# Performance work log

Hardware: AMD Instinct MI355X
Metric: run time of the kernel (lower is better)

## Reference

```python
import jax, jax.numpy as jnp
import numpy as np
from jax import lax

OC, IC, K = 256, 256, 3
PAD, STRIDE = 1, 1
NNZ = 59000
N, H, W = 32, 56, 56


def setup_inputs() -> dict:
    key = jax.random.key(0)
    k1, k2, k3, k4 = jax.random.split(key, 4)
    x = jax.random.normal(k1, (N, IC, H, W), dtype=jnp.float32)
    W_val = jax.random.normal(k2, (NNZ,), dtype=jnp.float32)
    W_idx = jax.random.randint(k3, (NNZ,), 0, OC * IC * K * K, dtype=jnp.int64)
    bias = jax.random.normal(k4, (OC,), dtype=jnp.float32)
    return {"x": x, "W_val": W_val, "W_idx": W_idx, "bias": bias}


def reference(x, W_val, W_idx, bias):
    # Scatter COO values into the dense [OC, IC, K, K] weight (duplicates sum).
    dense_w = jnp.zeros((OC * IC * K * K,), dtype=W_val.dtype).at[W_idx].add(W_val)
    dense_w = dense_w.reshape(OC, IC, K, K)
    # conv2d, NCHW / OIHW layout, stride=STRIDE, symmetric padding=PAD
    out = lax.conv_general_dilated(
        x, dense_w,
        window_strides=(STRIDE, STRIDE),
        padding=[(PAD, PAD), (PAD, PAD)],
        dimension_numbers=("NCHW", "OIHW", "NCHW"),
    )
    out = out + bias[None, :, None, None]
    return out
```

## Files before the change

### kernel.cpp

```cpp
#include <hip/hip_runtime.h>

typedef unsigned short ushort;
typedef __attribute__((ext_vector_type(8))) short bf16x8;
typedef __attribute__((ext_vector_type(4))) float f32x4;
typedef __attribute__((ext_vector_type(4))) ushort us4;

#define NBATCH 32
#define ICN 256
#define OCN 256
#define HSZ 56
#define WSZ 56
#define HP 58
#define SPAT (HP*HP)
#define KTOT 2304
#define MTOT (NBATCH*HSZ*WSZ)
#define NT   (KTOT/64)

#define XP_BYTES ((size_t)NBATCH*SPAT*ICN*2)
#define WD_BYTES ((size_t)OCN*KTOT*4)

__device__ __forceinline__ ushort f2bf(float f) {
  union { float f; unsigned u; } c; c.f = f;
  unsigned r = c.u + 0x7FFFu + ((c.u >> 16) & 1u);
  return (ushort)(r >> 16);
}

__global__ void k_transpose(const float* __restrict__ x, ushort* __restrict__ xp) {
  __shared__ ushort t2[WSZ*264];
  int h = blockIdx.x, n = blockIdx.y;
  ushort* dst = xp + ((size_t)n*SPAT + (size_t)h*HP)*ICN;
  if (h == 0 || h == HP-1) {
    for (int e = threadIdx.x; e < HP*ICN/4; e += 256) ((us4*)dst)[e] = (us4){0,0,0,0};
    return;
  }
  const float* src = x + ((size_t)n*ICN*HSZ*WSZ) + (size_t)(h-1)*WSZ;
  for (int e = threadIdx.x; e < ICN*WSZ; e += 256) {
    int ic = e / WSZ, w = e - ic*WSZ;
    t2[w*264 + ic] = f2bf(src[(size_t)ic*(HSZ*WSZ) + w]);
  }
  __syncthreads();
  for (int e4 = threadIdx.x; e4 < HP*ICN/4; e4 += 256) {
    int wp = e4 >> 6, ic4 = (e4 & 63) << 2;
    us4 v = (wp == 0 || wp == HP-1) ? (us4){0,0,0,0}
                                    : *(const us4*)&t2[(wp-1)*264 + ic4];
    ((us4*)dst)[e4] = v;
  }
}

__global__ void k_scatter(const int* __restrict__ idx, const float* __restrict__ val,
                          float* __restrict__ wd, int nnz) {
  int i = blockIdx.x*256 + threadIdx.x;
  if (i >= nnz) return;
  int id = idx[i];
  int oc = id / (ICN*9);
  int rem = id - oc*(ICN*9);
  int ic = rem / 9;
  int k9 = rem - ic*9;
  atomicAdd(wd + (size_t)oc*KTOT + k9*ICN + ic, val[i]);
}

__global__ void k_convert3(const float* __restrict__ wd, ushort* __restrict__ bm3) {
  int e = blockIdx.x*256 + threadIdx.x;
  int lam = e & 63;
  int f   = (e >> 6) & 3;
  int wc  = (e >> 8) & 3;
  int kh  = (e >> 10) & 1;
  int t   = e >> 11;
  int oc  = wc*64 + f*16 + (lam & 15);
  int k   = (t >> 2)*256 + (t & 3)*64 + kh*32 + (lam >> 4)*8;
  const float* src = wd + (size_t)oc*KTOT + k;
  float4 v0 = *(const float4*)(src);
  float4 v1 = *(const float4*)(src + 4);
  us4 lo, hi;
  lo[0]=f2bf(v0.x); lo[1]=f2bf(v0.y); lo[2]=f2bf(v0.z); lo[3]=f2bf(v0.w);
  hi[0]=f2bf(v1.x); hi[1]=f2bf(v1.y); hi[2]=f2bf(v1.z); hi[3]=f2bf(v1.w);
  ushort* dst = bm3 + (size_t)e*8;
  *(us4*)(dst) = lo; *(us4*)(dst+4) = hi;
}


#define GLD(gsrc, ldst) __builtin_amdgcn_global_load_lds( \
    (const __attribute__((address_space(1))) void*)(gsrc), \
    (__attribute__((address_space(3))) void*)(ldst), 16, 0, 0)
#define BAR()  asm volatile("s_barrier" ::: "memory")
#define VMW(N) do { asm volatile("s_waitcnt vmcnt(" #N ")" ::: "memory"); \
                    __builtin_amdgcn_sched_barrier(0); } while (0)
#define LGKM(N) do { asm volatile("s_waitcnt lgkmcnt(" #N ")" ::: "memory"); \
                     __builtin_amdgcn_sched_barrier(0); } while (0)

#define STAGE_AU(T1, U, BF) do { \
    const int t4_ = (T1) >> 2; const int khh_ = t4_/3, khw_ = t4_ - khh_*3; \
    const int koff_ = (khh_*HP + khw_)*256 + (((T1) & 3) << 6); \
    ushort* d_ = &Ab[(BF)*16384 + (U)*8192]; \
    GLD(xp + ((U) ? srcA10 : srcA00) + koff_, d_ + ldsOff0); \
    GLD(xp + ((U) ? srcA11 : srcA01) + koff_, d_ + ldsOff1); } while (0)

#define GLB(DST, VOFF) \
    asm volatile("global_load_dwordx4 %0, %4, %5 offset:0\n\t" \
                 "global_load_dwordx4 %1, %4, %5 offset:1024\n\t" \
                 "global_load_dwordx4 %2, %4, %5 offset:2048\n\t" \
                 "global_load_dwordx4 %3, %4, %5 offset:3072" \
                 : "=&v"(DST[0]), "=&v"(DST[1]), "=&v"(DST[2]), "=&v"(DST[3]) \
                 : "v"(VOFF), "s"(bm3) : "memory")

#define LOADA_TO(DST, KH, MH, BFB) do { \
    unsigned a_ = ((KH) ? aL1v : aL0v) + (unsigned)((BFB) + (MH)*8192); \
    asm volatile("ds_read_b128 %0, %4 offset:0\n\t" \
                 "ds_read_b128 %1, %4 offset:2048\n\t" \
                 "ds_read_b128 %2, %4 offset:4096\n\t" \
                 "ds_read_b128 %3, %4 offset:6144" \
                 : "=&v"(DST[0]), "=&v"(DST[1]), "=&v"(DST[2]), "=&v"(DST[3]) \
                 : "v"(a_)); } while (0)

#define MFMA16(MH, AV, BV) do { \
    __builtin_amdgcn_s_setprio(1); \
    _Pragma("unroll") \
    for (int f_ = 0; f_ < 4; ++f_) { \
      _Pragma("unroll") \
      for (int n_ = 0; n_ < 4; ++n_) \
        acc[(MH)*4+f_][n_] = __builtin_amdgcn_mfma_f32_16x16x32_bf16( \
            AV[f_], BV[n_], acc[(MH)*4+f_][n_], 0, 0, 0); \
    } \
    __builtin_amdgcn_s_setprio(0); } while (0)

__global__ __launch_bounds__(512, 2) void k_gemm8(const ushort* __restrict__ xp,
                                                  const ushort* __restrict__ bm3,
                                                  const float* __restrict__ bias,
                                                  float* __restrict__ out) {
  __shared__ __align__(128) ushort Ab[3*16384];

  const int tid = threadIdx.x;
  const int lam = tid & 63;
  const int wv  = tid >> 6;
  const int wr  = wv >> 2;
  const int wc  = wv & 3;
  const int la  = lam & 15;
  const int m0  = blockIdx.x * 256;

  const unsigned AbB = (unsigned)(uintptr_t)(__attribute__((address_space(3))) char*)Ab;

  const int q0 = (lam >> 4) ^ (la & 7);
  const unsigned aL0v = AbB + wr*16384 + la*128 + q0*16;
  const unsigned aL1v = AbB + wr*16384 + la*128 + (q0 ^ 4)*16;

  const unsigned wcB = wc*4096 + lam*16;

  const int ldsOff0 = (0*8 + wv)*512;
  const int ldsOff1 = (1*8 + wv)*512;
  int srcA00, srcA01, srcA10, srcA11;
  {
    const int oA = (lam & 7) ^ (lam >> 3);
    int m, n, rem, oh, ow, r;
    r = (0*8 + wv)*8 + (lam >> 3);
    m = m0 + 0*128 + r; n = m/3136; rem = m - n*3136; oh = rem/56; ow = rem - oh*56;
    srcA00 = (n*SPAT + oh*HP + ow)*ICN + oA*8;
    r = (1*8 + wv)*8 + (lam >> 3);
    m = m0 + 0*128 + r; n = m/3136; rem = m - n*3136; oh = rem/56; ow = rem - oh*56;
    srcA01 = (n*SPAT + oh*HP + ow)*ICN + oA*8;
    r = (0*8 + wv)*8 + (lam >> 3);
    m = m0 + 1*128 + r; n = m/3136; rem = m - n*3136; oh = rem/56; ow = rem - oh*56;
    srcA10 = (n*SPAT + oh*HP + ow)*ICN + oA*8;
    r = (1*8 + wv)*8 + (lam >> 3);
    m = m0 + 1*128 + r; n = m/3136; rem = m - n*3136; oh = rem/56; ow = rem - oh*56;
    srcA11 = (n*SPAT + oh*HP + ow)*ICN + oA*8;
  }

  f32x4 acc[8][4];
#pragma unroll
  for (int a = 0; a < 8; ++a)
#pragma unroll
    for (int b = 0; b < 4; ++b) acc[a][b] = (f32x4){0.f, 0.f, 0.f, 0.f};

  bf16x8 avq0_[4], avq1_[4], avq2_[4], avq3_[4], bvA_[4], bvB_[4];

  STAGE_AU(0, 0, 0); STAGE_AU(0, 1, 0);
  STAGE_AU(1, 0, 1); STAGE_AU(1, 1, 1);
  GLB(bvA_, wcB);
  VMW(4);
  BAR();
  LOADA_TO(avq0_, 0, 0, 0); LOADA_TO(avq1_, 0, 1, 0);

  int bf0 = 0, bf1 = 1, bf2 = 2;
  for (int t = 0; t < NT-2; ++t) {
    const int b0b = bf0*32768, b1b = bf1*32768;
    const unsigned vb = (unsigned)t*32768 + wcB;
    LOADA_TO(avq2_, 1, 0, b0b);
    GLB(bvB_, vb + 16384);
    VMW(4);
    LGKM(8);
    MFMA16(0, avq0_, bvA_);
    LOADA_TO(avq3_, 1, 1, b0b);
    STAGE_AU(t+2, 0, bf2);
    LGKM(8);
    MFMA16(1, avq1_, bvA_);
    BAR();
    LOADA_TO(avq0_, 0, 0, b1b);
    STAGE_AU(t+2, 1, bf2);
    VMW(4);
    LGKM(8);
    MFMA16(0, avq2_, bvB_);
    LOADA_TO(avq1_, 0, 1, b1b);
    GLB(bvA_, vb + 32768);
    LGKM(8);
    MFMA16(1, avq3_, bvB_);
    BAR();
    int bt = bf0; bf0 = bf1; bf1 = bf2; bf2 = bt;
  }

  {
    const int t = NT-2;
    const int b0b = bf0*32768, b1b = bf1*32768;
    const unsigned vb = (unsigned)t*32768 + wcB;
    LOADA_TO(avq2_, 1, 0, b0b);
    GLB(bvB_, vb + 16384);
    VMW(4);
    LGKM(8);
    MFMA16(0, avq0_, bvA_);
    LOADA_TO(avq3_, 1, 1, b0b);
    LGKM(8);
    MFMA16(1, avq1_, bvA_);
    BAR();
    LOADA_TO(avq0_, 0, 0, b1b);
    VMW(0);
    LGKM(8);
    MFMA16(0, avq2_, bvB_);
    LOADA_TO(avq1_, 0, 1, b1b);
    GLB(bvA_, vb + 32768);
    LGKM(8);
    MFMA16(1, avq3_, bvB_);
    BAR();
    int bt = bf0; bf0 = bf1; bf1 = bf2; bf2 = bt;
  }

  {
    const int t = NT-1;
    const int b0b = bf0*32768;
    const unsigned vb = (unsigned)t*32768 + wcB;
    LOADA_TO(avq2_, 1, 0, b0b);
    GLB(bvB_, vb + 16384);
    VMW(4);
    LGKM(8);
    MFMA16(0, avq0_, bvA_);
    LOADA_TO(avq3_, 1, 1, b0b);
    LGKM(8);
    MFMA16(1, avq1_, bvA_);
    VMW(0);
    LGKM(4);
    MFMA16(0, avq2_, bvB_);
    LGKM(0);
    MFMA16(1, avq3_, bvB_);
  }

#pragma unroll
  for (int nn = 0; nn < 4; ++nn) {
    int oc = wc*64 + nn*16 + la;
    float bvs = bias[oc];
#pragma unroll
    for (int mf = 0; mf < 8; ++mf) {
      int m = m0 + wr*128 + mf*16 + ((lam >> 4) << 2);
      int n = m / 3136;
      int rem = m - n*3136;
      float4 o;
      o.x = acc[mf][nn][0] + bvs;
      o.y = acc[mf][nn][1] + bvs;
      o.z = acc[mf][nn][2] + bvs;
      o.w = acc[mf][nn][3] + bvs;
      *(float4*)(out + ((size_t)(n*OCN + oc))*3136 + rem) = o;
    }
  }
}

extern "C" void kernel_launch(void* const* d_in, const int* in_sizes, int n_in,
                              void* d_out, int out_size, void* d_ws, size_t ws_size,
                              hipStream_t stream) {
  const float* x    = (const float*)d_in[0];
  const float* wval = (const float*)d_in[1];
  const int*   widx = (const int*)d_in[2];
  const float* bias = (const float*)d_in[3];
  float* out = (float*)d_out;
  const int nnz = in_sizes[1];

  char* ws = (char*)d_ws;
  ushort* xp  = (ushort*)ws;
  float*  wd  = (float*)(ws + XP_BYTES);
  ushort* bm3 = (ushort*)(ws + XP_BYTES + WD_BYTES);

  hipMemsetAsync(wd, 0, WD_BYTES, stream);
  k_transpose<<<dim3(HP, NBATCH), 256, 0, stream>>>(x, xp);
  k_scatter<<<dim3((nnz + 255)/256), 256, 0, stream>>>(widx, wval, wd, nnz);
  k_convert3<<<dim3((NT*2*16*64)/256), 256, 0, stream>>>(wd, bm3);
  k_gemm8<<<dim3(MTOT/256), 512, 0, stream>>>(xp, bm3, bias, out);
}
```

Baseline: 160.3 us.

## Switch GEMM inner loop from 16x16x32 to 32x32x16 bf16 MFMA tiles

Replaces the 16x16x32 MFMA micro-tiles with 32x32x16 MFMA instructions. This changes the weight pre-pack layout, the LDS staging layout (no XOR swizzle now), the A/B fragment loads and the epilogue store mapping. Larger MFMA tiles raise the compute per operand fetched and issue fewer instructions. The unswizzled LDS layout may cause bank conflicts on the ds_read_b128 fragment reads.

```diff
diff --git a/kernel.cpp b/kernel.cpp
--- a/kernel.cpp
+++ b/kernel.cpp
@@ -2,7 +2,7 @@
 
 typedef unsigned short ushort;
 typedef __attribute__((ext_vector_type(8))) short bf16x8;
-typedef __attribute__((ext_vector_type(4))) float f32x4;
+typedef __attribute__((ext_vector_type(16))) float f32x16;
 typedef __attribute__((ext_vector_type(4))) ushort us4;
 
 #define NBATCH 32
@@ -59,22 +59,21 @@
   atomicAdd(wd + (size_t)oc*KTOT + k9*ICN + ic, val[i]);
 }
 
-__global__ void k_convert3(const float* __restrict__ wd, ushort* __restrict__ bm3) {
+__global__ void k_convert4(const float* __restrict__ wd, ushort* __restrict__ bm4) {
   int e = blockIdx.x*256 + threadIdx.x;
-  int lam = e & 63;
-  int f   = (e >> 6) & 3;
-  int wc  = (e >> 8) & 3;
-  int kh  = (e >> 10) & 1;
-  int t   = e >> 11;
-  int oc  = wc*64 + f*16 + (lam & 15);
-  int k   = (t >> 2)*256 + (t & 3)*64 + kh*32 + (lam >> 4)*8;
+  int lam   = e & 63;
+  int nsubg = (e >> 6) & 7;
+  int ks    = (e >> 9) & 3;
+  int t     = e >> 11;
+  int oc = nsubg*32 + (lam & 31);
+  int k  = (t >> 2)*256 + (t & 3)*64 + ks*16 + (lam >> 5)*8;
   const float* src = wd + (size_t)oc*KTOT + k;
   float4 v0 = *(const float4*)(src);
   float4 v1 = *(const float4*)(src + 4);
   us4 lo, hi;
   lo[0]=f2bf(v0.x); lo[1]=f2bf(v0.y); lo[2]=f2bf(v0.z); lo[3]=f2bf(v0.w);
   hi[0]=f2bf(v1.x); hi[1]=f2bf(v1.y); hi[2]=f2bf(v1.z); hi[3]=f2bf(v1.w);
-  ushort* dst = bm3 + (size_t)e*8;
+  ushort* dst = bm4 + (size_t)e*8;
   *(us4*)(dst) = lo; *(us4*)(dst+4) = hi;
 }
 
@@ -88,43 +87,39 @@
 #define LGKM(N) do { asm volatile("s_waitcnt lgkmcnt(" #N ")" ::: "memory"); \
                      __builtin_amdgcn_sched_barrier(0); } while (0)
 
-#define STAGE_AU(T1, U, BF) do { \
-    const int t4_ = (T1) >> 2; const int khh_ = t4_/3, khw_ = t4_ - khh_*3; \
-    const int koff_ = (khh_*HP + khw_)*256 + (((T1) & 3) << 6); \
-    ushort* d_ = &Ab[(BF)*16384 + (U)*8192]; \
-    GLD(xp + ((U) ? srcA10 : srcA00) + koff_, d_ + ldsOff0); \
-    GLD(xp + ((U) ? srcA11 : srcA01) + koff_, d_ + ldsOff1); } while (0)
-
-#define GLB(DST, VOFF) \
-    asm volatile("global_load_dwordx4 %0, %4, %5 offset:0\n\t" \
-                 "global_load_dwordx4 %1, %4, %5 offset:1024\n\t" \
-                 "global_load_dwordx4 %2, %4, %5 offset:2048\n\t" \
-                 "global_load_dwordx4 %3, %4, %5 offset:3072" \
-                 : "=&v"(DST[0]), "=&v"(DST[1]), "=&v"(DST[2]), "=&v"(DST[3]) \
-                 : "v"(VOFF), "s"(bm3) : "memory")
-
-#define LOADA_TO(DST, KH, MH, BFB) do { \
-    unsigned a_ = ((KH) ? aL1v : aL0v) + (unsigned)((BFB) + (MH)*8192); \
+#define STAGE2(T2, HALF, B2B) do { \
+    const int t4_ = (T2) >> 2; const int khh_ = t4_/3, khw_ = t4_ - khh_*3; \
+    const int koff_ = (khh_*HP + khw_)*256 + (((T2) & 3) << 6); \
+    ushort* d_ = (ushort*)((char*)Ab + (B2B)); \
+    GLD(xp + ((HALF) ? sA2 : sA0) + koff_, d_ + dOffB + (HALF)*1024); \
+    GLD(xp + ((HALF) ? sA3 : sA1) + koff_, d_ + dOffB + (HALF)*1024 + 512); } while (0)
+
+#define GLB2(D0, D1, VOFF) \
+    asm volatile("global_load_dwordx4 %0, %2, %3 offset:0\n\t" \
+                 "global_load_dwordx4 %1, %2, %3 offset:1024" \
+                 : "=&v"(D0), "=&v"(D1) \
+                 : "v"(VOFF), "s"(bm4) : "memory")
+
+#define LOADA(DST, KS, BFB) do { \
+    unsigned a_ = aBase + (unsigned)((BFB) + (KS)*4096); \
     asm volatile("ds_read_b128 %0, %4 offset:0\n\t" \
-                 "ds_read_b128 %1, %4 offset:2048\n\t" \
-                 "ds_read_b128 %2, %4 offset:4096\n\t" \
-                 "ds_read_b128 %3, %4 offset:6144" \
+                 "ds_read_b128 %1, %4 offset:1024\n\t" \
+                 "ds_read_b128 %2, %4 offset:2048\n\t" \
+                 "ds_read_b128 %3, %4 offset:3072" \
                  : "=&v"(DST[0]), "=&v"(DST[1]), "=&v"(DST[2]), "=&v"(DST[3]) \
                  : "v"(a_)); } while (0)
 
-#define MFMA16(MH, AV, BV) do { \
+#define MFMA32B(AVQ, B0, B1) do { \
     __builtin_amdgcn_s_setprio(1); \
     _Pragma("unroll") \
-    for (int f_ = 0; f_ < 4; ++f_) { \
-      _Pragma("unroll") \
-      for (int n_ = 0; n_ < 4; ++n_) \
-        acc[(MH)*4+f_][n_] = __builtin_amdgcn_mfma_f32_16x16x32_bf16( \
-            AV[f_], BV[n_], acc[(MH)*4+f_][n_], 0, 0, 0); \
+    for (int m_ = 0; m_ < 4; ++m_) { \
+      acc[m_*2+0] = __builtin_amdgcn_mfma_f32_32x32x16_bf16(AVQ[m_], B0, acc[m_*2+0], 0, 0, 0); \
+      acc[m_*2+1] = __builtin_amdgcn_mfma_f32_32x32x16_bf16(AVQ[m_], B1, acc[m_*2+1], 0, 0, 0); \
     } \
     __builtin_amdgcn_s_setprio(0); } while (0)
 
 __global__ __launch_bounds__(512, 2) void k_gemm8(const ushort* __restrict__ xp,
-                                                  const ushort* __restrict__ bm3,
+                                                  const ushort* __restrict__ bm4,
                                                   const float* __restrict__ bias,
                                                   float* __restrict__ out) {
   __shared__ __align__(128) ushort Ab[3*16384];
@@ -134,138 +129,136 @@
   const int wv  = tid >> 6;
   const int wr  = wv >> 2;
   const int wc  = wv & 3;
-  const int la  = lam & 15;
   const int m0  = blockIdx.x * 256;
 
   const unsigned AbB = (unsigned)(uintptr_t)(__attribute__((address_space(3))) char*)Ab;
 
-  const int q0 = (lam >> 4) ^ (la & 7);
-  const unsigned aL0v = AbB + wr*16384 + la*128 + q0*16;
-  const unsigned aL1v = AbB + wr*16384 + la*128 + (q0 ^ 4)*16;
-
-  const unsigned wcB = wc*4096 + lam*16;
-
-  const int ldsOff0 = (0*8 + wv)*512;
-  const int ldsOff1 = (1*8 + wv)*512;
-  int srcA00, srcA01, srcA10, srcA11;
+  const unsigned aBase = AbB + wr*16384 + lam*16;
+  const unsigned wcB = wc*2048 + lam*16;
+
+  const int dOffB = ((wv >> 2)*16 + (wv & 3)*4)*512;
+  int sA0, sA1, sA2, sA3;
   {
-    const int oA = (lam & 7) ^ (lam >> 3);
-    int m, n, rem, oh, ow, r;
-    r = (0*8 + wv)*8 + (lam >> 3);
-    m = m0 + 0*128 + r; n = m/3136; rem = m - n*3136; oh = rem/56; ow = rem - oh*56;
-    srcA00 = (n*SPAT + oh*HP + ow)*ICN + oA*8;
-    r = (1*8 + wv)*8 + (lam >> 3);
-    m = m0 + 0*128 + r; n = m/3136; rem = m - n*3136; oh = rem/56; ow = rem - oh*56;
-    srcA01 = (n*SPAT + oh*HP + ow)*ICN + oA*8;
-    r = (0*8 + wv)*8 + (lam >> 3);
-    m = m0 + 1*128 + r; n = m/3136; rem = m - n*3136; oh = rem/56; ow = rem - oh*56;
-    srcA10 = (n*SPAT + oh*HP + ow)*ICN + oA*8;
-    r = (1*8 + wv)*8 + (lam >> 3);
-    m = m0 + 1*128 + r; n = m/3136; rem = m - n*3136; oh = rem/56; ow = rem - oh*56;
-    srcA11 = (n*SPAT + oh*HP + ow)*ICN + oA*8;
-  }
-
-  f32x4 acc[8][4];
-#pragma unroll
-  for (int a = 0; a < 8; ++a)
-#pragma unroll
-    for (int b = 0; b < 4; ++b) acc[a][b] = (f32x4){0.f, 0.f, 0.f, 0.f};
-
-  bf16x8 avq0_[4], avq1_[4], avq2_[4], avq3_[4], bvA_[4], bvB_[4];
-
-  STAGE_AU(0, 0, 0); STAGE_AU(0, 1, 0);
-  STAGE_AU(1, 0, 1); STAGE_AU(1, 1, 1);
-  GLB(bvA_, wcB);
-  VMW(4);
+    const int kpart = (wv & 3)*16 + (lam >> 5)*8;
+    int m, n, rem, oh, ow;
+    m = m0 + (wv >> 2)*128 + 0*32 + (lam & 31);
+    n = m/3136; rem = m - n*3136; oh = rem/56; ow = rem - oh*56;
+    sA0 = (n*SPAT + oh*HP + ow)*ICN + kpart;
+    m = m0 + (wv >> 2)*128 + 1*32 + (lam & 31);
+    n = m/3136; rem = m - n*3136; oh = rem/56; ow = rem - oh*56;
+    sA1 = (n*SPAT + oh*HP + ow)*ICN + kpart;
+    m = m0 + (wv >> 2)*128 + 2*32 + (lam & 31);
+    n = m/3136; rem = m - n*3136; oh = rem/56; ow = rem - oh*56;
+    sA2 = (n*SPAT + oh*HP + ow)*ICN + kpart;
+    m = m0 + (wv >> 2)*128 + 3*32 + (lam & 31);
+    n = m/3136; rem = m - n*3136; oh = rem/56; ow = rem - oh*56;
+    sA3 = (n*SPAT + oh*HP + ow)*ICN + kpart;
+  }
+
+  f32x16 acc[8];
+#pragma unroll
+  for (int a = 0; a < 8; ++a) acc[a] = (f32x16)(0.f);
+
+  bf16x8 avq0_[4], avq1_[4], avq2_[4], avq3_[4];
+  bf16x8 bA0_, bA1_, bA2_, bA3_, bB0_, bB1_, bB2_, bB3_;
+
+  STAGE2(0, 0, 0); STAGE2(0, 1, 0);
+  STAGE2(1, 0, 32768); STAGE2(1, 1, 32768);
+  GLB2(bA0_, bA1_, wcB);
+  GLB2(bA2_, bA3_, wcB + 8192);
+  VMW(8);
   BAR();
-  LOADA_TO(avq0_, 0, 0, 0); LOADA_TO(avq1_, 0, 1, 0);
-
-  int bf0 = 0, bf1 = 1, bf2 = 2;
+  LOADA(avq0_, 0, 0); LOADA(avq1_, 1, 0);
+
+  int bf0b = 0, bf1b = 32768, bf2b = 65536;
   for (int t = 0; t < NT-2; ++t) {
-    const int b0b = bf0*32768, b1b = bf1*32768;
     const unsigned vb = (unsigned)t*32768 + wcB;
-    LOADA_TO(avq2_, 1, 0, b0b);
-    GLB(bvB_, vb + 16384);
-    VMW(4);
-    LGKM(8);
-    MFMA16(0, avq0_, bvA_);
-    LOADA_TO(avq3_, 1, 1, b0b);
-    STAGE_AU(t+2, 0, bf2);
-    LGKM(8);
-    MFMA16(1, avq1_, bvA_);
-    BAR();
-    LOADA_TO(avq0_, 0, 0, b1b);
-    STAGE_AU(t+2, 1, bf2);
-    VMW(4);
-    LGKM(8);
-    MFMA16(0, avq2_, bvB_);
-    LOADA_TO(avq1_, 0, 1, b1b);
-    GLB(bvA_, vb + 32768);
-    LGKM(8);
-    MFMA16(1, avq3_, bvB_);
-    BAR();
-    int bt = bf0; bf0 = bf1; bf1 = bf2; bf2 = bt;
+    LOADA(avq2_, 2, bf0b);
+    GLB2(bB0_, bB1_, vb + 16384);
+    GLB2(bB2_, bB3_, vb + 24576);
+    VMW(4);
+    LGKM(8);
+    MFMA32B(avq0_, bA0_, bA1_);
+    LOADA(avq3_, 3, bf0b);
+    STAGE2(t+2, 0, bf2b);
+    LGKM(8);
+    MFMA32B(avq1_, bA2_, bA3_);
+    BAR();
+    LOADA(avq0_, 0, bf1b);
+    STAGE2(t+2, 1, bf2b);
+    VMW(4);
+    LGKM(8);
+    MFMA32B(avq2_, bB0_, bB1_);
+    LOADA(avq1_, 1, bf1b);
+    GLB2(bA0_, bA1_, vb + 32768);
+    GLB2(bA2_, bA3_, vb + 40960);
+    LGKM(8);
+    MFMA32B(avq3_, bB2_, bB3_);
+    BAR();
+    int bt = bf0b; bf0b = bf1b; bf1b = bf2b; bf2b = bt;
   }
 
   {
-    const int t = NT-2;
-    const int b0b = bf0*32768, b1b = bf1*32768;
-    const unsigned vb = (unsigned)t*32768 + wcB;
-    LOADA_TO(avq2_, 1, 0, b0b);
-    GLB(bvB_, vb + 16384);
-    VMW(4);
-    LGKM(8);
-    MFMA16(0, avq0_, bvA_);
-    LOADA_TO(avq3_, 1, 1, b0b);
-    LGKM(8);
-    MFMA16(1, avq1_, bvA_);
-    BAR();
-    LOADA_TO(avq0_, 0, 0, b1b);
+    const unsigned vb = (unsigned)(NT-2)*32768 + wcB;
+    LOADA(avq2_, 2, bf0b);
+    GLB2(bB0_, bB1_, vb + 16384);
+    GLB2(bB2_, bB3_, vb + 24576);
+    VMW(4);
+    LGKM(8);
+    MFMA32B(avq0_, bA0_, bA1_);
+    LOADA(avq3_, 3, bf0b);
+    LGKM(8);
+    MFMA32B(avq1_, bA2_, bA3_);
+    BAR();
+    LOADA(avq0_, 0, bf1b);
     VMW(0);
     LGKM(8);
-    MFMA16(0, avq2_, bvB_);
-    LOADA_TO(avq1_, 0, 1, b1b);
-    GLB(bvA_, vb + 32768);
-    LGKM(8);
-    MFMA16(1, avq3_, bvB_);
-    BAR();
-    int bt = bf0; bf0 = bf1; bf1 = bf2; bf2 = bt;
+    MFMA32B(avq2_, bB0_, bB1_);
+    LOADA(avq1_, 1, bf1b);
+    GLB2(bA0_, bA1_, vb + 32768);
+    GLB2(bA2_, bA3_, vb + 40960);
+    LGKM(8);
+    MFMA32B(avq3_, bB2_, bB3_);
+    BAR();
+    int bt = bf0b; bf0b = bf1b; bf1b = bf2b; bf2b = bt;
   }
 
   {
-    const int t = NT-1;
-    const int b0b = bf0*32768;
-    const unsigned vb = (unsigned)t*32768 + wcB;
-    LOADA_TO(avq2_, 1, 0, b0b);
-    GLB(bvB_, vb + 16384);
-    VMW(4);
-    LGKM(8);
-    MFMA16(0, avq0_, bvA_);
-    LOADA_TO(avq3_, 1, 1, b0b);
-    LGKM(8);
-    MFMA16(1, avq1_, bvA_);
+    const unsigned vb = (unsigned)(NT-1)*32768 + wcB;
+    LOADA(avq2_, 2, bf0b);
+    GLB2(bB0_, bB1_, vb + 16384);
+    GLB2(bB2_, bB3_, vb + 24576);
+    VMW(4);
+    LGKM(8);
+    MFMA32B(avq0_, bA0_, bA1_);
+    LOADA(avq3_, 3, bf0b);
+    LGKM(8);
+    MFMA32B(avq1_, bA2_, bA3_);
     VMW(0);
     LGKM(4);
-    MFMA16(0, avq2_, bvB_);
+    MFMA32B(avq2_, bB0_, bB1_);
     LGKM(0);
-    MFMA16(1, avq3_, bvB_);
-  }
-
-#pragma unroll
-  for (int nn = 0; nn < 4; ++nn) {
-    int oc = wc*64 + nn*16 + la;
-    float bvs = bias[oc];
-#pragma unroll
-    for (int mf = 0; mf < 8; ++mf) {
-      int m = m0 + wr*128 + mf*16 + ((lam >> 4) << 2);
-      int n = m / 3136;
-      int rem = m - n*3136;
-      float4 o;
-      o.x = acc[mf][nn][0] + bvs;
-      o.y = acc[mf][nn][1] + bvs;
-      o.z = acc[mf][nn][2] + bvs;
-      o.w = acc[mf][nn][3] + bvs;
-      *(float4*)(out + ((size_t)(n*OCN + oc))*3136 + rem) = o;
+    MFMA32B(avq3_, bB2_, bB3_);
+  }
+
+#pragma unroll
+  for (int ms = 0; ms < 4; ++ms) {
+#pragma unroll
+    for (int ns = 0; ns < 2; ++ns) {
+      int oc = wc*64 + ns*32 + (lam & 31);
+      float bvs = bias[oc];
+#pragma unroll
+      for (int q = 0; q < 4; ++q) {
+        int m = m0 + wr*128 + ms*32 + q*8 + ((lam >> 5) << 2);
+        int n = m / 3136;
+        int rem = m - n*3136;
+        float4 o;
+        o.x = acc[ms*2+ns][q*4+0] + bvs;
+        o.y = acc[ms*2+ns][q*4+1] + bvs;
+        o.z = acc[ms*2+ns][q*4+2] + bvs;
+        o.w = acc[ms*2+ns][q*4+3] + bvs;
+        *(float4*)(out + ((size_t)(n*OCN + oc))*3136 + rem) = o;
+      }
     }
   }
 }
@@ -283,11 +276,11 @@
   char* ws = (char*)d_ws;
   ushort* xp  = (ushort*)ws;
   float*  wd  = (float*)(ws + XP_BYTES);
-  ushort* bm3 = (ushort*)(ws + XP_BYTES + WD_BYTES);
+  ushort* bm4 = (ushort*)(ws + XP_BYTES + WD_BYTES);
 
   hipMemsetAsync(wd, 0, WD_BYTES, stream);
   k_transpose<<<dim3(HP, NBATCH), 256, 0, stream>>>(x, xp);
   k_scatter<<<dim3((nnz + 255)/256), 256, 0, stream>>>(widx, wval, wd, nnz);
-  k_convert3<<<dim3((NT*2*16*64)/256), 256, 0, stream>>>(wd, bm3);
-  k_gemm8<<<dim3(MTOT/256), 512, 0, stream>>>(xp, bm3, bias, out);
-}
+  k_convert4<<<dim3((NT*4*8*64)/256), 256, 0, stream>>>(wd, bm4);
+  k_gemm8<<<dim3(MTOT/256), 512, 0, stream>>>(xp, bm4, bias, out);
+}
```

After: 172.7 us. 1.08x slower.
